# Kernel optimization log

Measured on AMD Instinct MI355X. Metric: run time of the kernel, lower is better.

Reference implementation:

```python
import jax, jax.numpy as jnp
import numpy as np

B = 4
N_CPGS = 20000
N_FREQS = N_CPGS // 2 + 1  # rfft length
E = 320000
H = 4
HD = 16          # head_dim = graph_hidden // n_heads
GH = 64          # graph_hidden
FD = 64          # fusion_dim
FH = 128         # fft_hidden
PH = 128         # plasticity_hidden


def _ln(x, g, b, eps=1e-5):
    m = x.mean(-1, keepdims=True)
    v = ((x - m) ** 2).mean(-1, keepdims=True)
    return (x - m) / jnp.sqrt(v + eps) * g + b


def _gelu(x):
    return jax.nn.gelu(x, approximate=False)  # torch default: exact erf GELU


def setup_inputs() -> dict:
    key = jax.random.key(0)
    ki = iter(jax.random.split(key, 40))
    nrm = lambda shape, s=0.02: jax.random.normal(next(ki), shape, dtype=jnp.float32) * s
    z = lambda *s: jnp.zeros(s, jnp.float32)
    o = lambda *s: jnp.ones(s, jnp.float32)
    return dict(
        x=jax.random.uniform(next(ki), (B, N_CPGS), dtype=jnp.float32),
        edge_index=jax.random.randint(next(ki), (2, E), 0, N_CPGS, dtype=jnp.int32),
        fft_freq_weights=o(N_FREQS),
        fft_w1=nrm((FH, N_FREQS)), fft_b1=z(FH), fft_ln1_g=o(FH), fft_ln1_b=z(FH),
        fft_w2=nrm((FD, FH)), fft_b2=z(FD), fft_ln2_g=o(FD), fft_ln2_b=z(FD),
        ge_w=nrm((GH, 1)), ge_b=z(GH), ge_ln_g=o(GH), ge_ln_b=z(GH),
        gat_w=nrm((GH, GH)), gat_attn=nrm((H, 2 * HD), 0.1),
        gp_w=nrm((FD, GH)), gp_b=z(FD), gp_ln_g=o(FD), gp_ln_b=z(FD),
        pl_W=nrm((PH, N_FREQS), 0.01), pl_alpha=o(PH, N_FREQS) * 0.01,
        pl_eta=jnp.array([0.1], jnp.float32), pl_bias=z(PH),
        pn_g=o(PH), pn_b=z(PH),
        pp_w=nrm((FD, PH)), pp_b=z(FD), pp_ln_g=o(FD), pp_ln_b=z(FD),
        gate_w1=nrm((6, 3 * FD)), gate_b1=z(6), gate_w2=nrm((3, 6)), gate_b2=z(3),
        head_w1=nrm((32, FD)), head_b1=z(32), head_w2=nrm((1, 32)), head_b2=z(1),
    )


def reference(x, edge_index, fft_freq_weights,
              fft_w1, fft_b1, fft_ln1_g, fft_ln1_b, fft_w2, fft_b2, fft_ln2_g, fft_ln2_b,
              ge_w, ge_b, ge_ln_g, ge_ln_b, gat_w, gat_attn,
              gp_w, gp_b, gp_ln_g, gp_ln_b,
              pl_W, pl_alpha, pl_eta, pl_bias, pn_g, pn_b,
              pp_w, pp_b, pp_ln_g, pp_ln_b,
              gate_w1, gate_b1, gate_w2, gate_b2,
              head_w1, head_b1, head_w2, head_b2):
    Bsz, n = x.shape
    # ---- Stream 1: FFT ----
    xc = x - x.mean(axis=1, keepdims=True)
    mag = jnp.log1p(jnp.abs(jnp.fft.rfft(xc, axis=1)))          # (B, N_FREQS)
    freq_w = jax.nn.softmax(fft_freq_weights) * fft_freq_weights.shape[0]
    magw = mag * freq_w[None, :]
    f = _gelu(_ln(magw @ fft_w1.T + fft_b1, fft_ln1_g, fft_ln1_b))
    fft_feat = _ln(f @ fft_w2.T + fft_b2, fft_ln2_g, fft_ln2_b)  # (B, FD)
    # ---- Stream 2: sparse graph attention (eval: dropout off) ----
    h0 = _gelu(_ln(x[..., None] * ge_w[:, 0] + ge_b, ge_ln_g, ge_ln_b))  # (B, N, GH)
    h = (h0 @ gat_w.T).reshape(Bsz, n, H, HD)
    a_src, a_dst = gat_attn[:, :HD], gat_attn[:, HD:]
    s_src = jnp.einsum('bnhd,hd->bnh', h, a_src)
    s_dst = jnp.einsum('bnhd,hd->bnh', h, a_dst)
    src, dst = edge_index[0], edge_index[1]
    scores = s_src[:, src] + s_dst[:, dst]                       # (B, E, H)
    scores = jnp.where(scores >= 0, scores, 0.2 * scores)        # leaky_relu(0.2)
    # max with include_self=True over zero-init buffer (matches torch scatter_reduce)
    m = jnp.zeros((Bsz, n, H), scores.dtype).at[:, dst].max(scores)
    e = jnp.exp(scores - m[:, dst])
    ssum = jnp.zeros((Bsz, n, H), e.dtype).at[:, dst].add(e)
    attn = e / (ssum[:, dst] + 1e-8)
    msg = h[:, src] * attn[..., None]                            # (B, E, H, HD)
    gat_out = jnp.zeros((Bsz, n, H, HD), msg.dtype).at[:, dst].add(msg).reshape(Bsz, n, H * HD)
    hg = h0 + _gelu(gat_out)
    graph_feat = _ln(hg.mean(axis=1) @ gp_w.T + gp_b, gp_ln_g, gp_ln_b)  # (B, FD)
    # ---- Stream 3: Hebbian plastic layer on mag ----
    y_slow = mag @ pl_W.T + pl_bias                              # (B, PH)
    x_norm = mag / (jnp.linalg.norm(mag, axis=-1, keepdims=True) + 1e-8)
    y_pre = jnp.tanh(y_slow)
    # bmm(alpha * eta * outer(y_pre, x_norm), x) == eta * y_pre * ((x_norm*x) @ alpha.T)
    contrib = pl_eta[0] * y_pre * ((x_norm * mag) @ jax.nn.sigmoid(pl_alpha).T)
    plastic = _ln(_gelu(y_slow + contrib), pn_g, pn_b)
    plastic_feat = _ln(plastic @ pp_w.T + pp_b, pp_ln_g, pp_ln_b)
    # ---- Gated fusion ----
    concat = jnp.concatenate([fft_feat, graph_feat, plastic_feat], axis=-1)  # (B, 3*FD)
    g = _gelu(concat @ gate_w1.T + gate_b1) @ gate_w2.T + gate_b2
    gw = jax.nn.softmax(g, axis=-1)                              # (B, 3)
    fused = fft_feat * gw[:, 0:1] + graph_feat * gw[:, 1:2] + plastic_feat * gw[:, 2:3]
    # ---- Head ----
    out = _gelu(fused @ head_w1.T + head_b1) @ head_w2.T + head_b2
    return out.squeeze(-1)                                       # (B,)
```

## Files before the change

kernel.cpp:

```cpp
#include <hip/hip_runtime.h>
#include <math.h>

constexpr int N_CPGS = 20000;
constexpr int NF     = 10001;
constexpr int BZ     = 4;
constexpr int NEDGE  = 320000;
constexpr int KPAD   = 10240;
constexpr int FN1    = 200;
constexpr int FN2    = 100;
constexpr int NS2    = 4;
constexpr int TILES  = (N_CPGS + 63) / 64;
constexpr int HB     = NEDGE / 256;

constexpr size_t W_XMEAN   = 0;
constexpr size_t W_SMSTAT  = 64;
constexpr size_t W_NORMSQ  = 128;
constexpr size_t W_H0SUM   = 192;
constexpr size_t W_GATMEAN = 448;
constexpr size_t W_PREP    = 704;
constexpr size_t W_D       = 768;
constexpr size_t W_MAG     = 2304;
constexpr size_t W_SSRC    = 42368;
constexpr size_t W_SDST    = 362368;
constexpr size_t W_H       = 682368;
constexpr size_t W_Y       = 5802368;
constexpr size_t W_P2      = 5962368;
constexpr size_t W_COUNTS  = 9079168;
constexpr size_t W_OFFS    = 9099168;
constexpr size_t W_CURSOR  = 9119232;
constexpr size_t W_SORTSRC = 9139232;

#define DEVFN static __device__ __forceinline__

DEVFN float gelu_f(float v) {
    float ax = fabsf(v) * 0.70710678118654752440f;
    float t = 1.0f / fmaf(0.3275911f, ax, 1.0f);
    float p = fmaf(t, 1.061405429f, -1.453152027f);
    p = fmaf(p, t, 1.421413741f);
    p = fmaf(p, t, -0.284496736f);
    p = fmaf(p, t, 0.254829592f);
    p = p * t;
    float e = __expf(-ax * ax);
    float er = copysignf(fmaf(-p, e, 1.0f), v);
    return 0.5f * v * (1.0f + er);
}

DEVFN float wred_sum(float v) {
    #pragma unroll
    for (int m = 32; m; m >>= 1) v += __shfl_xor(v, m);
    return v;
}

DEVFN unsigned int bfr(float f) {
    unsigned int u = __float_as_uint(f);
    return (u + 0x7fffu + ((u >> 16) & 1u)) >> 16;
}
DEVFN float bf2f(unsigned short v) { return __uint_as_float(((unsigned int)v) << 16); }

__global__ void k_pre(const float* __restrict__ x, const float* __restrict__ ge_w,
                      const float* __restrict__ ge_b, const float* __restrict__ fw,
                      float* __restrict__ ws) {
    int bb = blockIdx.x, t = threadIdx.x;
    __shared__ float sd[256];
    if (bb < 4) {
        const float4* x4 = (const float4*)(x + (size_t)bb * N_CPGS);
        float s = 0.f;
        for (int i = t; i < N_CPGS / 4; i += 256) {
            float4 v = x4[i];
            s += (v.x + v.y) + (v.z + v.w);
        }
        sd[t] = s; __syncthreads();
        for (int o = 128; o; o >>= 1) { if (t < o) sd[t] += sd[t + o]; __syncthreads(); }
        if (t == 0) ws[W_XMEAN + bb] = sd[0] * (1.0f / N_CPGS);
    } else if (bb == 4) {
        for (int i = t; i < (int)(W_PREP - W_NORMSQ); i += 256) ws[W_NORMSQ + i] = 0.f;
        if (t < 64) {
            float w = ge_w[t], b = ge_b[t];
            float mw = wred_sum(w) * (1.f / 64.f);
            float mb = wred_sum(b) * (1.f / 64.f);
            float wc = w - mw, bc = b - mb;
            float A = wred_sum(wc * wc) * (1.f / 64.f);
            float C = wred_sum(wc * bc) * (1.f / 64.f);
            float D = wred_sum(bc * bc) * (1.f / 64.f);
            if (t == 0) { float* p = ws + W_PREP; p[0] = mw; p[1] = mb; p[2] = A; p[3] = C; p[4] = D; }
        }
    } else if (bb == 5) {
        float mx = -1e30f;
        for (int i = t; i < NF; i += 256) mx = fmaxf(mx, fw[i]);
        sd[t] = mx; __syncthreads();
        for (int o = 128; o; o >>= 1) { if (t < o) sd[t] = fmaxf(sd[t], sd[t + o]); __syncthreads(); }
        mx = sd[0]; __syncthreads();
        float s = 0.f;
        for (int i = t; i < NF; i += 256) s += expf(fw[i] - mx);
        sd[t] = s; __syncthreads();
        for (int o = 128; o; o >>= 1) { if (t < o) sd[t] += sd[t + o]; __syncthreads(); }
        if (t == 0) { ws[W_SMSTAT] = mx; ws[W_SMSTAT + 1] = sd[0]; }
    } else {
        int base = (bb - 6) * 1000;
        int* cnt = (int*)(ws + W_COUNTS);
        for (int i = t; i < 1000; i += 256) cnt[base + i] = 0;
    }
}

__global__ __launch_bounds__(256) void k_node(
    const float* __restrict__ x, const float* __restrict__ ge_w, const float* __restrict__ ge_b,
    const float* __restrict__ ge_g, const float* __restrict__ ge_beta,
    const float* __restrict__ gat_w, const float* __restrict__ gat_attn,
    const int* __restrict__ ei, float* __restrict__ ws)
{
    int t = threadIdx.x;
    int nb = blockIdx.x;
    if (nb >= 4 * TILES) {
        int r = nb - 4 * TILES;
        if (r < HB) {
            int e = r * 256 + t;
            if (e < NEDGE) atomicAdd((int*)(ws + W_COUNTS) + ei[NEDGE + e], 1);
        } else {
            int fb = r - HB;
            int b = fb / 100;
            int n1base = (fb % 100) * 2;
            int n1l = t >> 7, k2 = t & 127;
            __shared__ float xs[2][100];
            float xm = ws[W_XMEAN + b];
            for (int i = t; i < 200; i += 256) {
                int nl = (i >= 100) ? 1 : 0, n2 = (i >= 100) ? i - 100 : i;
                xs[nl][n2] = x[(size_t)b * N_CPGS + n1base + nl + 200 * n2] - xm;
            }
            __syncthreads();
            int k2e = (k2 < 100) ? k2 : 0;
            constexpr float T100 = 6.2831853071795864769f / 100.f;
            float dc, dsn;
            { float sn, cn; sincosf(T100 * (float)k2e, &sn, &cn); dc = cn; dsn = -sn; }
            float yr = 0.f, yi = 0.f;
            #pragma unroll
            for (int half = 0; half < 2; ++half) {
                float c, s;
                { int m = (k2e * (half * 50)) % 100; float sn, cn; sincosf(T100 * (float)m, &sn, &cn); c = cn; s = -sn; }
                #pragma unroll 5
                for (int j = 0; j < 50; ++j) {
                    float xv = xs[n1l][half * 50 + j];
                    yr = fmaf(xv, c, yr); yi = fmaf(xv, s, yi);
                    float tc_ = c * dc - s * dsn; s = s * dc + c * dsn; c = tc_;
                }
            }
            if (k2 < 100)
                ((float2*)(ws + W_Y))[((size_t)b * FN1 + n1base + n1l) * FN2 + k2] = make_float2(yr, yi);
        }
        return;
    }
    int b = nb / TILES;
    int tile = nb % TILES;
    int n0 = tile * 64;

    __shared__ __align__(16) float h0T[64 * 68];
    __shared__ __align__(16) float gwT[64 * 68];
    __shared__ float xsv[64], rss[64];

    const float* prep = ws + W_PREP;
    float mw = prep[0], mb = prep[1], A = prep[2], C = prep[3], Dd = prep[4];

    for (int idx = t; idx < 4096; idx += 256) { int i = idx >> 6, j = idx & 63; gwT[j * 68 + i] = gat_w[idx]; }
    if (t < 64) {
        int n = n0 + t;
        float xv = (n < N_CPGS) ? x[(size_t)b * N_CPGS + n] : 0.f;
        xsv[t] = xv;
        float var = xv * xv * A + 2.f * xv * C + Dd;
        rss[t] = 1.0f / sqrtf(var + 1e-5f);
    }
    __syncthreads();

    for (int idx = t; idx < 4096; idx += 256) {
        int j = idx >> 6, nd = idx & 63;
        float h0 = 0.f;
        if (n0 + nd < N_CPGS) {
            float v = (xsv[nd] * (ge_w[j] - mw) + (ge_b[j] - mb)) * rss[nd];
            h0 = gelu_f(v * ge_g[j] + ge_beta[j]);
        }
        h0T[j * 68 + nd] = h0;
    }
    __syncthreads();

    int tr = t >> 4, tc = t & 15;
    float acc[4][4] = {};
    #pragma unroll 8
    for (int j = 0; j < 64; ++j) {
        const float4 av = *(const float4*)&h0T[j * 68 + (tr << 2)];
        const float4 bv = *(const float4*)&gwT[j * 68 + (tc << 2)];
        #pragma unroll
        for (int u = 0; u < 4; ++u) {
            float a = (u == 0) ? av.x : (u == 1) ? av.y : (u == 2) ? av.z : av.w;
            acc[u][0] = fmaf(a, bv.x, acc[u][0]);
            acc[u][1] = fmaf(a, bv.y, acc[u][1]);
            acc[u][2] = fmaf(a, bv.z, acc[u][2]);
            acc[u][3] = fmaf(a, bv.w, acc[u][3]);
        }
    }
    if (t < 64) {
        float s = 0.f;
        #pragma unroll 8
        for (int nd = 0; nd < 64; ++nd) s += h0T[t * 68 + nd];
        atomicAdd(ws + W_H0SUM + b * 64 + t, s);
    }
    unsigned short* hb = (unsigned short*)(ws + W_H);
    #pragma unroll
    for (int u = 0; u < 4; ++u) {
        int n = n0 + tr * 4 + u;
        if (n < N_CPGS) {
            unsigned int lo = bfr(acc[u][0]) | (bfr(acc[u][1]) << 16);
            unsigned int hi = bfr(acc[u][2]) | (bfr(acc[u][3]) << 16);
            *(uint2*)(hb + ((size_t)b * N_CPGS + n) * 64 + tc * 4) = make_uint2(lo, hi);
        }
    }
    __syncthreads();
    #pragma unroll
    for (int u = 0; u < 4; ++u)
        *(float4*)&h0T[(tr * 4 + u) * 68 + tc * 4] =
            make_float4(acc[u][0], acc[u][1], acc[u][2], acc[u][3]);
    __syncthreads();
    if (t < 64) {
        int n = n0 + t;
        if (n < N_CPGS) {
            #pragma unroll
            for (int hh = 0; hh < 4; ++hh) {
                float as = 0.f, ad = 0.f;
                #pragma unroll
                for (int d = 0; d < 16; ++d) {
                    float hv = h0T[t * 68 + hh * 16 + d];
                    as = fmaf(hv, gat_attn[hh * 32 + d], as);
                    ad = fmaf(hv, gat_attn[hh * 32 + 16 + d], ad);
                }
                ws[W_SSRC + ((size_t)b * N_CPGS + n) * 4 + hh] = as;
                ws[W_SDST + ((size_t)b * N_CPGS + n) * 4 + hh] = ad;
            }
        }
    }
}

__global__ __launch_bounds__(1024) void k_sf2(float* __restrict__ ws) {
    int t = threadIdx.x;
    if (blockIdx.x == 0) {
        const int* cnt = (const int*)(ws + W_COUNTS);
        int* offs = (int*)(ws + W_OFFS);
        int* cur  = (int*)(ws + W_CURSOR);
        int i0 = t * 20;
        int s = 0;
        for (int i = 0; i < 20; ++i) { int idx = i0 + i; if (idx < N_CPGS) s += cnt[idx]; }
        __shared__ int sd[1024];
        sd[t] = s; __syncthreads();
        for (int off = 1; off < 1024; off <<= 1) {
            int v = (t >= off) ? sd[t - off] : 0;
            __syncthreads();
            sd[t] += v;
            __syncthreads();
        }
        int run = sd[t] - s;
        for (int i = 0; i < 20; ++i) {
            int idx = i0 + i;
            if (idx < N_CPGS) { offs[idx] = run; cur[idx] = run; run += cnt[idx]; }
        }
        if (t == 1023) offs[N_CPGS] = sd[1023];
        return;
    }
    int kb = blockIdx.x - 1;
    int ns = t >> 8;
    int k = kb * 256 + (t & 255);
    int n1b = ns * 50;
    int k2 = k % 100;
    const float2* Y2 = (const float2*)(ws + W_Y);
    constexpr float W0 = 6.2831853071795864769f / 20000.f;
    float dc, dsn;
    { float sn, cn; sincosf(W0 * (float)k, &sn, &cn); dc = cn; dsn = -sn; }
    float c, s;
    { int m = (k * n1b) % 20000; float sn, cn; sincosf(W0 * (float)m, &sn, &cn); c = cn; s = -sn; }
    float xr0 = 0.f, xi0 = 0.f, xr1 = 0.f, xi1 = 0.f;
    float xr2 = 0.f, xi2 = 0.f, xr3 = 0.f, xi3 = 0.f;
    #pragma unroll 5
    for (int j = 0; j < 50; ++j) {
        int n1 = n1b + j;
        float2 y0 = Y2[(0 * FN1 + (size_t)n1) * FN2 + k2];
        float2 y1 = Y2[(1 * FN1 + (size_t)n1) * FN2 + k2];
        float2 y2 = Y2[(2 * FN1 + (size_t)n1) * FN2 + k2];
        float2 y3 = Y2[(3 * FN1 + (size_t)n1) * FN2 + k2];
        xr0 = fmaf(y0.x, c, xr0); xr0 = fmaf(-y0.y, s, xr0);
        xi0 = fmaf(y0.x, s, xi0); xi0 = fmaf( y0.y, c, xi0);
        xr1 = fmaf(y1.x, c, xr1); xr1 = fmaf(-y1.y, s, xr1);
        xi1 = fmaf(y1.x, s, xi1); xi1 = fmaf( y1.y, c, xi1);
        xr2 = fmaf(y2.x, c, xr2); xr2 = fmaf(-y2.y, s, xr2);
        xi2 = fmaf(y2.x, s, xi2); xi2 = fmaf( y2.y, c, xi2);
        xr3 = fmaf(y3.x, c, xr3); xr3 = fmaf(-y3.y, s, xr3);
        xi3 = fmaf(y3.x, s, xi3); xi3 = fmaf( y3.y, c, xi3);
        float tc_ = c * dc - s * dsn; s = s * dc + c * dsn; c = tc_;
    }
    float* p = ws + W_P2 + ((size_t)ns * KPAD + k) * 8;
    p[0] = xr0; p[1] = xi0; p[2] = xr1; p[3] = xi1;
    p[4] = xr2; p[5] = xi2; p[6] = xr3; p[7] = xi3;
}

__global__ __launch_bounds__(256) void k_scatmagr(const int* __restrict__ ei,
                                                  float* __restrict__ ws) {
    int t = threadIdx.x;
    if (blockIdx.x < HB) {
        int e = blockIdx.x * 256 + t;
        if (e < NEDGE) {
            int s = ei[e], d = ei[NEDGE + e];
            int pos = atomicAdd((int*)(ws + W_CURSOR) + d, 1);
            ((int*)(ws + W_SORTSRC))[pos] = s;
        }
        return;
    }
    int gid = (blockIdx.x - HB) * 256 + t;
    bool ok = gid < BZ * NF;
    int b = ok ? gid / NF : 0;
    int k = ok ? gid - b * NF : 0;
    float m = 0.f;
    if (ok) {
        float re = 0.f, im = 0.f;
        const float* p = ws + W_P2 + (size_t)k * 8 + b * 2;
        #pragma unroll
        for (int ns = 0; ns < NS2; ++ns) { re += p[0]; im += p[1]; p += (size_t)KPAD * 8; }
        m = log1pf(sqrtf(re * re + im * im));
        ws[W_MAG + (size_t)b * NF + k] = m;
    }
    float msq = ok ? m * m : 0.f;
    #pragma unroll
    for (int bb = 0; bb < 4; ++bb) {
        float v = (ok && b == bb) ? msq : 0.f;
        v = wred_sum(v);
        if ((t & 63) == 0) atomicAdd(ws + W_NORMSQ + bb, v);
    }
}

__global__ __launch_bounds__(256) void k_gatdots(
    const float* __restrict__ fftw1, const float* __restrict__ plW,
    const float* __restrict__ plalpha, const float* __restrict__ fw,
    float* __restrict__ ws)
{
    int t = threadIdx.x;
    if (blockIdx.x < 2048) {
        int xcd = blockIdx.x & 7;
        int b = xcd >> 1;
        int blk = ((blockIdx.x >> 3) << 1) | (xcd & 1);
        int w = t >> 6, lane = t & 63;
        int wv = blk * 4 + w;
        int egrp = lane >> 4, fgrp = lane & 15;
        int hh = fgrp >> 2;
        const int* offs = (const int*)(ws + W_OFFS);
        const int* ssrt = (const int*)(ws + W_SORTSRC);
        const float4* s4src = (const float4*)(ws + W_SSRC);
        const float4* s4dst = (const float4*)(ws + W_SDST);
        const unsigned short* hb = (const unsigned short*)(ws + W_H);
        size_t bN = (size_t)b * N_CPGS;
        float gacc0 = 0.f, gacc1 = 0.f, gacc2 = 0.f, gacc3 = 0.f;

        __shared__ float elds[4][4][68];
        __shared__ int   slds[4][68];

        for (int dst = wv; dst < N_CPGS; dst += 2048) {
            int o0 = offs[dst], o1 = offs[dst + 1];
            if (o0 == o1) continue;
            float4 sd4 = s4dst[bN + dst];
            float p0 = 0.f, p1 = 0.f, p2 = 0.f, p3 = 0.f;
            float a0 = 0.f, a1 = 0.f, a2 = 0.f, a3 = 0.f;
            for (int c0 = o0; c0 < o1; c0 += 64) {
                int cnt = min(64, o1 - c0);
                float v0 = 0.f, v1 = 0.f, v2 = 0.f, v3 = 0.f;
                int s = 0;
                if (lane < cnt) {
                    s = ssrt[c0 + lane];
                    float4 ss = s4src[bN + s];
                    v0 = ss.x + sd4.x; v0 = (v0 >= 0.f) ? v0 : 0.2f * v0; v0 = __expf(v0);
                    v1 = ss.y + sd4.y; v1 = (v1 >= 0.f) ? v1 : 0.2f * v1; v1 = __expf(v1);
                    v2 = ss.z + sd4.z; v2 = (v2 >= 0.f) ? v2 : 0.2f * v2; v2 = __expf(v2);
                    v3 = ss.w + sd4.w; v3 = (v3 >= 0.f) ? v3 : 0.2f * v3; v3 = __expf(v3);
                }
                slds[w][lane] = s;
                elds[w][0][lane] = v0; elds[w][1][lane] = v1;
                elds[w][2][lane] = v2; elds[w][3][lane] = v3;
                p0 += v0; p1 += v1; p2 += v2; p3 += v3;
                int niter = (cnt + 3) >> 2;
                for (int i = 0; i < niter; ++i) {
                    int j = i * 4 + egrp;
                    float e = elds[w][hh][j];
                    int sj = slds[w][j];
                    uint2 hv = *(const uint2*)(hb + (((size_t)(bN + sj)) << 6) + (fgrp << 2));
                    a0 = fmaf(e, bf2f((unsigned short)(hv.x & 0xffffu)), a0);
                    a1 = fmaf(e, bf2f((unsigned short)(hv.x >> 16)), a1);
                    a2 = fmaf(e, bf2f((unsigned short)(hv.y & 0xffffu)), a2);
                    a3 = fmaf(e, bf2f((unsigned short)(hv.y >> 16)), a3);
                }
            }
            float q0 = wred_sum(p0), q1 = wred_sum(p1), q2 = wred_sum(p2), q3 = wred_sum(p3);
            float ssum = (hh == 0) ? q0 : (hh == 1) ? q1 : (hh == 2) ? q2 : q3;
            a0 += __shfl_xor(a0, 16); a0 += __shfl_xor(a0, 32);
            a1 += __shfl_xor(a1, 16); a1 += __shfl_xor(a1, 32);
            a2 += __shfl_xor(a2, 16); a2 += __shfl_xor(a2, 32);
            a3 += __shfl_xor(a3, 16); a3 += __shfl_xor(a3, 32);
            float inv = 1.f / (ssum + 1e-8f);
            gacc0 += gelu_f(a0 * inv); gacc1 += gelu_f(a1 * inv);
            gacc2 += gelu_f(a2 * inv); gacc3 += gelu_f(a3 * inv);
        }
        __shared__ float gred[4][64];
        if (egrp == 0) {
            gred[w][fgrp * 4 + 0] = gacc0; gred[w][fgrp * 4 + 1] = gacc1;
            gred[w][fgrp * 4 + 2] = gacc2; gred[w][fgrp * 4 + 3] = gacc3;
        }
        __syncthreads();
        if (t < 64)
            atomicAdd(ws + W_GATMEAN + b * 64 + t, gred[0][t] + gred[1][t] + gred[2][t] + gred[3][t]);
        return;
    }
    int bb2 = blockIdx.x - 2048;
    int m = bb2 >> 7;
    int r = bb2 & 127;
    const float* mag = ws + W_MAG;
    float smx = ws[W_SMSTAT], ssm = ws[W_SMSTAT + 1];
    float sc_fw = (float)NF / ssm;
    float inv_n0 = 1.f / (sqrtf(ws[W_NORMSQ + 0]) + 1e-8f);
    float inv_n1 = 1.f / (sqrtf(ws[W_NORMSQ + 1]) + 1e-8f);
    float inv_n2 = 1.f / (sqrtf(ws[W_NORMSQ + 2]) + 1e-8f);
    float inv_n3 = 1.f / (sqrtf(ws[W_NORMSQ + 3]) + 1e-8f);
    const float* row = ((m == 0) ? fftw1 : (m == 1) ? plW : plalpha) + (size_t)r * NF;
    float a0 = 0.f, a1 = 0.f, a2 = 0.f, a3 = 0.f;
    for (int k = t; k < NF; k += 256) {
        float wv = row[k];
        float g0 = mag[k], g1 = mag[NF + k], g2 = mag[2 * NF + k], g3 = mag[3 * NF + k];
        if (m == 0) {
            float s = expf(fw[k] - smx) * sc_fw;
            wv *= s;
            a0 = fmaf(wv, g0, a0); a1 = fmaf(wv, g1, a1); a2 = fmaf(wv, g2, a2); a3 = fmaf(wv, g3, a3);
        } else if (m == 1) {
            a0 = fmaf(wv, g0, a0); a1 = fmaf(wv, g1, a1); a2 = fmaf(wv, g2, a2); a3 = fmaf(wv, g3, a3);
        } else {
            wv = 1.f / (1.f + expf(-wv));
            a0 = fmaf(wv, g0 * g0 * inv_n0, a0); a1 = fmaf(wv, g1 * g1 * inv_n1, a1);
            a2 = fmaf(wv, g2 * g2 * inv_n2, a2); a3 = fmaf(wv, g3 * g3 * inv_n3, a3);
        }
    }
    __shared__ float sd[256];
    float acc[4] = {a0, a1, a2, a3};
    #pragma unroll
    for (int bb = 0; bb < 4; ++bb) {
        sd[t] = acc[bb]; __syncthreads();
        for (int o = 128; o; o >>= 1) { if (t < o) sd[t] += sd[t + o]; __syncthreads(); }
        if (t == 0) ws[W_D + ((size_t)m * 128 + r) * 4 + bb] = sd[0];
        __syncthreads();
    }
}

DEVFN float ln64(float v, const float* g, const float* bt, int lane) {
    float mn = wred_sum(v) * (1.f / 64.f);
    float d = v - mn;
    float var = wred_sum(d * d) * (1.f / 64.f);
    return d * (1.0f / sqrtf(var + 1e-5f)) * g[lane] + bt[lane];
}
DEVFN void ln128(float& v0, float& v1, const float* g, const float* bt, int lane) {
    float mn = wred_sum(v0 + v1) * (1.f / 128.f);
    float d0 = v0 - mn, d1 = v1 - mn;
    float var = wred_sum(d0 * d0 + d1 * d1) * (1.f / 128.f);
    float rs = 1.0f / sqrtf(var + 1e-5f);
    v0 = d0 * rs * g[lane] + bt[lane];
    v1 = d1 * rs * g[lane + 64] + bt[lane + 64];
}
DEVFN float dotW128(const float* __restrict__ W, const float* __restrict__ v, int c) {
    const float4* w4 = (const float4*)(W + (size_t)c * 128);
    float acc = 0.f;
    #pragma unroll
    for (int q = 0; q < 32; ++q) {
        float4 wv = w4[q];
        const float* vv = v + q * 4;
        acc = fmaf(wv.x, vv[0], acc); acc = fmaf(wv.y, vv[1], acc);
        acc = fmaf(wv.z, vv[2], acc); acc = fmaf(wv.w, vv[3], acc);
    }
    return acc;
}
DEVFN float dotW64(const float* __restrict__ W, const float* __restrict__ v, int c) {
    const float4* w4 = (const float4*)(W + (size_t)c * 64);
    float acc = 0.f;
    #pragma unroll
    for (int q = 0; q < 16; ++q) {
        float4 wv = w4[q];
        const float* vv = v + q * 4;
        acc = fmaf(wv.x, vv[0], acc); acc = fmaf(wv.y, vv[1], acc);
        acc = fmaf(wv.z, vv[2], acc); acc = fmaf(wv.w, vv[3], acc);
    }
    return acc;
}

__global__ __launch_bounds__(256) void k_final(
    const float* __restrict__ fft_b1, const float* __restrict__ fft_ln1_g, const float* __restrict__ fft_ln1_b,
    const float* __restrict__ fft_w2, const float* __restrict__ fft_b2,
    const float* __restrict__ fft_ln2_g, const float* __restrict__ fft_ln2_b,
    const float* __restrict__ gp_w, const float* __restrict__ gp_b,
    const float* __restrict__ gp_ln_g, const float* __restrict__ gp_ln_b,
    const float* __restrict__ pl_eta, const float* __restrict__ pl_bias,
    const float* __restrict__ pn_g, const float* __restrict__ pn_b,
    const float* __restrict__ pp_w, const float* __restrict__ pp_b,
    const float* __restrict__ pp_ln_g, const float* __restrict__ pp_ln_b,
    const float* __restrict__ gate_w1, const float* __restrict__ gate_b1,
    const float* __restrict__ gate_w2, const float* __restrict__ gate_b2,
    const float* __restrict__ head_w1, const float* __restrict__ head_b1,
    const float* __restrict__ head_w2, const float* __restrict__ head_b2,
    float* __restrict__ ws, float* __restrict__ out)
{
    int t = threadIdx.x, b = t >> 6, lane = t & 63;
    __shared__ float vlds[4][256];
    float* vb = vlds[b];
    const float* D = ws + W_D;
    int r0 = lane, r1 = lane + 64;

    float f0 = D[(0 * 128 + r0) * 4 + b] + fft_b1[r0];
    float f1 = D[(0 * 128 + r1) * 4 + b] + fft_b1[r1];
    ln128(f0, f1, fft_ln1_g, fft_ln1_b, lane);
    vb[lane] = gelu_f(f0); vb[64 + lane] = gelu_f(f1);
    float catf = ln64(dotW128(fft_w2, vb, lane) + fft_b2[lane], fft_ln2_g, fft_ln2_b, lane);

    float hgm = (ws[W_H0SUM + b * 64 + lane] + ws[W_GATMEAN + b * 64 + lane]) * (1.f / N_CPGS);
    vb[lane] = hgm;
    float catg = ln64(dotW64(gp_w, vb, lane) + gp_b[lane], gp_ln_g, gp_ln_b, lane);

    float eta = pl_eta[0];
    float ys0 = D[(1 * 128 + r0) * 4 + b] + pl_bias[r0];
    float ys1 = D[(1 * 128 + r1) * 4 + b] + pl_bias[r1];
    float q0 = D[(2 * 128 + r0) * 4 + b];
    float q1 = D[(2 * 128 + r1) * 4 + b];
    float u0 = gelu_f(ys0 + eta * tanhf(ys0) * q0);
    float u1 = gelu_f(ys1 + eta * tanhf(ys1) * q1);
    ln128(u0, u1, pn_g, pn_b, lane);
    vb[lane] = u0; vb[64 + lane] = u1;
    float catp = ln64(dotW128(pp_w, vb, lane) + pp_b[lane], pp_ln_g, pp_ln_b, lane);

    vb[lane] = catf; vb[64 + lane] = catg; vb[128 + lane] = catp;
    if (lane < 6) {
        float a = gate_b1[lane];
        const float* wrow = gate_w1 + lane * 192;
        #pragma unroll 4
        for (int j = 0; j < 192; ++j) a = fmaf(wrow[j], vb[j], a);
        vb[192 + lane] = gelu_f(a);
    }
    float gv[3];
    #pragma unroll
    for (int c = 0; c < 3; ++c) {
        float a = gate_b2[c];
        #pragma unroll
        for (int j = 0; j < 6; ++j) a = fmaf(gate_w2[c * 6 + j], vb[192 + j], a);
        gv[c] = a;
    }
    float gmx = fmaxf(gv[0], fmaxf(gv[1], gv[2]));
    float e0 = expf(gv[0] - gmx), e1 = expf(gv[1] - gmx), e2 = expf(gv[2] - gmx);
    float inv = 1.f / (e0 + e1 + e2);
    float fus = catf * (e0 * inv) + catg * (e1 * inv) + catp * (e2 * inv);

    vb[lane] = fus;
    float hval = 0.f;
    if (lane < 32) {
        float a = dotW64(head_w1, vb, lane) + head_b1[lane];
        hval = gelu_f(a) * head_w2[lane];
    }
    float o = wred_sum(hval);
    if (lane == 0) out[b] = o + head_b2[0];
}

extern "C" void kernel_launch(void* const* d_in, const int* in_sizes, int n_in,
                              void* d_out, int out_size, void* d_ws, size_t ws_size,
                              hipStream_t stream) {
    (void)in_sizes; (void)n_in; (void)out_size; (void)ws_size;
    const float* x        = (const float*)d_in[0];
    const int*   ei       = (const int*)d_in[1];
    const float* fw       = (const float*)d_in[2];
    const float* fft_w1   = (const float*)d_in[3];
    const float* fft_b1   = (const float*)d_in[4];
    const float* fft_ln1g = (const float*)d_in[5];
    const float* fft_ln1b = (const float*)d_in[6];
    const float* fft_w2   = (const float*)d_in[7];
    const float* fft_b2   = (const float*)d_in[8];
    const float* fft_ln2g = (const float*)d_in[9];
    const float* fft_ln2b = (const float*)d_in[10];
    const float* ge_w     = (const float*)d_in[11];
    const float* ge_b     = (const float*)d_in[12];
    const float* ge_g     = (const float*)d_in[13];
    const float* ge_beta  = (const float*)d_in[14];
    const float* gat_w    = (const float*)d_in[15];
    const float* gat_attn = (const float*)d_in[16];
    const float* gp_w     = (const float*)d_in[17];
    const float* gp_b     = (const float*)d_in[18];
    const float* gp_ln_g  = (const float*)d_in[19];
    const float* gp_ln_b  = (const float*)d_in[20];
    const float* pl_W     = (const float*)d_in[21];
    const float* pl_alpha = (const float*)d_in[22];
    const float* pl_eta   = (const float*)d_in[23];
    const float* pl_bias  = (const float*)d_in[24];
    const float* pn_g     = (const float*)d_in[25];
    const float* pn_b     = (const float*)d_in[26];
    const float* pp_w     = (const float*)d_in[27];
    const float* pp_b     = (const float*)d_in[28];
    const float* pp_ln_g  = (const float*)d_in[29];
    const float* pp_ln_b  = (const float*)d_in[30];
    const float* gate_w1  = (const float*)d_in[31];
    const float* gate_b1  = (const float*)d_in[32];
    const float* gate_w2  = (const float*)d_in[33];
    const float* gate_b2  = (const float*)d_in[34];
    const float* head_w1  = (const float*)d_in[35];
    const float* head_b1  = (const float*)d_in[36];
    const float* head_w2  = (const float*)d_in[37];
    const float* head_b2  = (const float*)d_in[38];

    float* ws  = (float*)d_ws;
    float* out = (float*)d_out;

    k_pre<<<26, 256, 0, stream>>>(x, ge_w, ge_b, fw, ws);
    k_node<<<4 * TILES + HB + 400, 256, 0, stream>>>(x, ge_w, ge_b, ge_g, ge_beta,
                                                     gat_w, gat_attn, ei, ws);
    k_sf2<<<41, 1024, 0, stream>>>(ws);
    k_scatmagr<<<HB + (BZ * NF + 255) / 256, 256, 0, stream>>>(ei, ws);
    k_gatdots<<<2048 + 384, 256, 0, stream>>>(fft_w1, pl_W, pl_alpha, fw, ws);
    k_final<<<1, 256, 0, stream>>>(fft_b1, fft_ln1g, fft_ln1b, fft_w2, fft_b2, fft_ln2g, fft_ln2b,
                                   gp_w, gp_b, gp_ln_g, gp_ln_b, pl_eta, pl_bias, pn_g, pn_b,
                                   pp_w, pp_b, pp_ln_g, pp_ln_b, gate_w1, gate_b1, gate_w2, gate_b2,
                                   head_w1, head_b1, head_w2, head_b2, ws, out);
}
```

Before: 213.9 us.

## Interleave batch dimension in node/FFT buffers and process all batches per GAT destination

Changes the layouts of the FFT intermediate Y, the bf16 node features H and the attention scores so the batch index is innermost. This lets the second FFT stage read all four batches with two float4 loads and the GAT aggregation handle all four batches per destination in one pass. Edge indices and the softmax setup are then shared across batches instead of repeated. The attention score dot products are now computed from registers with lane shuffles instead of a shared-memory round trip. The FFT second stage is split over eight n1 segments with twice the blocks. The price is much higher register use per GAT thread and fewer GAT blocks.

```diff
diff --git a/kernel.cpp b/kernel.cpp
--- a/kernel.cpp
+++ b/kernel.cpp
@@ -8,9 +8,10 @@
 constexpr int KPAD   = 10240;
 constexpr int FN1    = 200;
 constexpr int FN2    = 100;
-constexpr int NS2    = 4;
+constexpr int NS2    = 8;
 constexpr int TILES  = (N_CPGS + 63) / 64;
 constexpr int HB     = NEDGE / 256;
+constexpr int GATB   = 1024;
 
 constexpr size_t W_XMEAN   = 0;
 constexpr size_t W_SMSTAT  = 64;
@@ -144,7 +145,7 @@
                 }
             }
             if (k2 < 100)
-                ((float2*)(ws + W_Y))[((size_t)b * FN1 + n1base + n1l) * FN2 + k2] = make_float2(yr, yi);
+                ((float2*)(ws + W_Y))[((size_t)(n1base + n1l) * FN2 + k2) * 4 + b] = make_float2(yr, yi);
         }
         return;
     }
@@ -201,36 +202,44 @@
         for (int nd = 0; nd < 64; ++nd) s += h0T[t * 68 + nd];
         atomicAdd(ws + W_H0SUM + b * 64 + t, s);
     }
-    unsigned short* hb = (unsigned short*)(ws + W_H);
+    unsigned short* hbp = (unsigned short*)(ws + W_H);
     #pragma unroll
     for (int u = 0; u < 4; ++u) {
         int n = n0 + tr * 4 + u;
         if (n < N_CPGS) {
             unsigned int lo = bfr(acc[u][0]) | (bfr(acc[u][1]) << 16);
             unsigned int hi = bfr(acc[u][2]) | (bfr(acc[u][3]) << 16);
-            *(uint2*)(hb + ((size_t)b * N_CPGS + n) * 64 + tc * 4) = make_uint2(lo, hi);
-        }
-    }
-    __syncthreads();
-    #pragma unroll
-    for (int u = 0; u < 4; ++u)
-        *(float4*)&h0T[(tr * 4 + u) * 68 + tc * 4] =
-            make_float4(acc[u][0], acc[u][1], acc[u][2], acc[u][3]);
-    __syncthreads();
-    if (t < 64) {
-        int n = n0 + t;
-        if (n < N_CPGS) {
+            *(uint2*)(hbp + ((size_t)n * 4 + b) * 64 + tc * 4) = make_uint2(lo, hi);
+        }
+    }
+    {
+        int hh = tc >> 2;
+        float ps[4], pd[4];
+        #pragma unroll
+        for (int u = 0; u < 4; ++u) {
+            float s = 0.f, d = 0.f;
             #pragma unroll
-            for (int hh = 0; hh < 4; ++hh) {
-                float as = 0.f, ad = 0.f;
-                #pragma unroll
-                for (int d = 0; d < 16; ++d) {
-                    float hv = h0T[t * 68 + hh * 16 + d];
-                    as = fmaf(hv, gat_attn[hh * 32 + d], as);
-                    ad = fmaf(hv, gat_attn[hh * 32 + 16 + d], ad);
+            for (int kk = 0; kk < 4; ++kk) {
+                float asv = gat_attn[hh * 32 + (tc & 3) * 4 + kk];
+                float adv = gat_attn[hh * 32 + 16 + (tc & 3) * 4 + kk];
+                s = fmaf(acc[u][kk], asv, s);
+                d = fmaf(acc[u][kk], adv, d);
+            }
+            ps[u] = s; pd[u] = d;
+        }
+        #pragma unroll
+        for (int u = 0; u < 4; ++u) {
+            ps[u] += __shfl_xor(ps[u], 1); ps[u] += __shfl_xor(ps[u], 2);
+            pd[u] += __shfl_xor(pd[u], 1); pd[u] += __shfl_xor(pd[u], 2);
+        }
+        if ((tc & 3) == 0) {
+            #pragma unroll
+            for (int u = 0; u < 4; ++u) {
+                int n = n0 + tr * 4 + u;
+                if (n < N_CPGS) {
+                    ws[W_SSRC + ((size_t)n * 4 + b) * 4 + hh] = ps[u];
+                    ws[W_SDST + ((size_t)n * 4 + b) * 4 + hh] = pd[u];
                 }
-                ws[W_SSRC + ((size_t)b * N_CPGS + n) * 4 + hh] = as;
-                ws[W_SDST + ((size_t)b * N_CPGS + n) * 4 + hh] = ad;
             }
         }
     }
@@ -261,12 +270,13 @@
         if (t == 1023) offs[N_CPGS] = sd[1023];
         return;
     }
-    int kb = blockIdx.x - 1;
-    int ns = t >> 8;
+    int bb = blockIdx.x - 1;
+    int kb = bb >> 1;
+    int ns = (bb & 1) * 4 + (t >> 8);
     int k = kb * 256 + (t & 255);
-    int n1b = ns * 50;
+    int n1b = ns * 25;
     int k2 = k % 100;
-    const float2* Y2 = (const float2*)(ws + W_Y);
+    const float4* Yp = (const float4*)(ws + W_Y);
     constexpr float W0 = 6.2831853071795864769f / 20000.f;
     float dc, dsn;
     { float sn, cn; sincosf(W0 * (float)k, &sn, &cn); dc = cn; dsn = -sn; }
@@ -275,20 +285,17 @@
     float xr0 = 0.f, xi0 = 0.f, xr1 = 0.f, xi1 = 0.f;
     float xr2 = 0.f, xi2 = 0.f, xr3 = 0.f, xi3 = 0.f;
     #pragma unroll 5
-    for (int j = 0; j < 50; ++j) {
-        int n1 = n1b + j;
-        float2 y0 = Y2[(0 * FN1 + (size_t)n1) * FN2 + k2];
-        float2 y1 = Y2[(1 * FN1 + (size_t)n1) * FN2 + k2];
-        float2 y2 = Y2[(2 * FN1 + (size_t)n1) * FN2 + k2];
-        float2 y3 = Y2[(3 * FN1 + (size_t)n1) * FN2 + k2];
-        xr0 = fmaf(y0.x, c, xr0); xr0 = fmaf(-y0.y, s, xr0);
-        xi0 = fmaf(y0.x, s, xi0); xi0 = fmaf( y0.y, c, xi0);
-        xr1 = fmaf(y1.x, c, xr1); xr1 = fmaf(-y1.y, s, xr1);
-        xi1 = fmaf(y1.x, s, xi1); xi1 = fmaf( y1.y, c, xi1);
-        xr2 = fmaf(y2.x, c, xr2); xr2 = fmaf(-y2.y, s, xr2);
-        xi2 = fmaf(y2.x, s, xi2); xi2 = fmaf( y2.y, c, xi2);
-        xr3 = fmaf(y3.x, c, xr3); xr3 = fmaf(-y3.y, s, xr3);
-        xi3 = fmaf(y3.x, s, xi3); xi3 = fmaf( y3.y, c, xi3);
+    for (int j = 0; j < 25; ++j) {
+        size_t base = ((size_t)(n1b + j) * FN2 + k2) * 2;
+        float4 y01 = Yp[base], y23 = Yp[base + 1];
+        xr0 = fmaf(y01.x, c, xr0); xr0 = fmaf(-y01.y, s, xr0);
+        xi0 = fmaf(y01.x, s, xi0); xi0 = fmaf( y01.y, c, xi0);
+        xr1 = fmaf(y01.z, c, xr1); xr1 = fmaf(-y01.w, s, xr1);
+        xi1 = fmaf(y01.z, s, xi1); xi1 = fmaf( y01.w, c, xi1);
+        xr2 = fmaf(y23.x, c, xr2); xr2 = fmaf(-y23.y, s, xr2);
+        xi2 = fmaf(y23.x, s, xi2); xi2 = fmaf( y23.y, c, xi2);
+        xr3 = fmaf(y23.z, c, xr3); xr3 = fmaf(-y23.w, s, xr3);
+        xi3 = fmaf(y23.z, s, xi3); xi3 = fmaf( y23.w, c, xi3);
         float tc_ = c * dc - s * dsn; s = s * dc + c * dsn; c = tc_;
     }
     float* p = ws + W_P2 + ((size_t)ns * KPAD + k) * 8;
@@ -336,80 +343,106 @@
     float* __restrict__ ws)
 {
     int t = threadIdx.x;
-    if (blockIdx.x < 2048) {
-        int xcd = blockIdx.x & 7;
-        int b = xcd >> 1;
-        int blk = ((blockIdx.x >> 3) << 1) | (xcd & 1);
+    if (blockIdx.x < GATB) {
         int w = t >> 6, lane = t & 63;
-        int wv = blk * 4 + w;
+        int wv = blockIdx.x * 4 + w;
         int egrp = lane >> 4, fgrp = lane & 15;
         int hh = fgrp >> 2;
         const int* offs = (const int*)(ws + W_OFFS);
         const int* ssrt = (const int*)(ws + W_SORTSRC);
         const float4* s4src = (const float4*)(ws + W_SSRC);
         const float4* s4dst = (const float4*)(ws + W_SDST);
-        const unsigned short* hb = (const unsigned short*)(ws + W_H);
-        size_t bN = (size_t)b * N_CPGS;
-        float gacc0 = 0.f, gacc1 = 0.f, gacc2 = 0.f, gacc3 = 0.f;
-
-        __shared__ float elds[4][4][68];
+        const uint2* hbp = (const uint2*)(ws + W_H);
+        float gacc[4][4] = {};
+
+        __shared__ float elds[4][4][4][68];
         __shared__ int   slds[4][68];
-
-        for (int dst = wv; dst < N_CPGS; dst += 2048) {
+        __shared__ float gred[4][4][64];
+
+        for (int dst = wv; dst < N_CPGS; dst += 4 * GATB) {
             int o0 = offs[dst], o1 = offs[dst + 1];
             if (o0 == o1) continue;
-            float4 sd4 = s4dst[bN + dst];
-            float p0 = 0.f, p1 = 0.f, p2 = 0.f, p3 = 0.f;
-            float a0 = 0.f, a1 = 0.f, a2 = 0.f, a3 = 0.f;
+            float4 sd4[4];
+            #pragma unroll
+            for (int b = 0; b < 4; ++b) sd4[b] = s4dst[(size_t)dst * 4 + b];
+            float av[4][4] = {};
+            float es[4] = {};
             for (int c0 = o0; c0 < o1; c0 += 64) {
                 int cnt = min(64, o1 - c0);
-                float v0 = 0.f, v1 = 0.f, v2 = 0.f, v3 = 0.f;
                 int s = 0;
-                if (lane < cnt) {
-                    s = ssrt[c0 + lane];
-                    float4 ss = s4src[bN + s];
-                    v0 = ss.x + sd4.x; v0 = (v0 >= 0.f) ? v0 : 0.2f * v0; v0 = __expf(v0);
-                    v1 = ss.y + sd4.y; v1 = (v1 >= 0.f) ? v1 : 0.2f * v1; v1 = __expf(v1);
-                    v2 = ss.z + sd4.z; v2 = (v2 >= 0.f) ? v2 : 0.2f * v2; v2 = __expf(v2);
-                    v3 = ss.w + sd4.w; v3 = (v3 >= 0.f) ? v3 : 0.2f * v3; v3 = __expf(v3);
+                if (lane < cnt) s = ssrt[c0 + lane];
+                slds[w][lane] = s;
+                #pragma unroll
+                for (int b = 0; b < 4; ++b) {
+                    float v0 = 0.f, v1 = 0.f, v2 = 0.f, v3 = 0.f;
+                    if (lane < cnt) {
+                        float4 ss = s4src[(size_t)s * 4 + b];
+                        v0 = ss.x + sd4[b].x; v0 = (v0 >= 0.f) ? v0 : 0.2f * v0; v0 = __expf(v0);
+                        v1 = ss.y + sd4[b].y; v1 = (v1 >= 0.f) ? v1 : 0.2f * v1; v1 = __expf(v1);
+                        v2 = ss.z + sd4[b].z; v2 = (v2 >= 0.f) ? v2 : 0.2f * v2; v2 = __expf(v2);
+                        v3 = ss.w + sd4[b].w; v3 = (v3 >= 0.f) ? v3 : 0.2f * v3; v3 = __expf(v3);
+                    }
+                    elds[w][b][0][lane] = v0; elds[w][b][1][lane] = v1;
+                    elds[w][b][2][lane] = v2; elds[w][b][3][lane] = v3;
                 }
-                slds[w][lane] = s;
-                elds[w][0][lane] = v0; elds[w][1][lane] = v1;
-                elds[w][2][lane] = v2; elds[w][3][lane] = v3;
-                p0 += v0; p1 += v1; p2 += v2; p3 += v3;
                 int niter = (cnt + 3) >> 2;
                 for (int i = 0; i < niter; ++i) {
-                    int j = i * 4 + egrp;
-                    float e = elds[w][hh][j];
+                    int j = (i << 2) + egrp;
                     int sj = slds[w][j];
-                    uint2 hv = *(const uint2*)(hb + (((size_t)(bN + sj)) << 6) + (fgrp << 2));
-                    a0 = fmaf(e, bf2f((unsigned short)(hv.x & 0xffffu)), a0);
-                    a1 = fmaf(e, bf2f((unsigned short)(hv.x >> 16)), a1);
-                    a2 = fmaf(e, bf2f((unsigned short)(hv.y & 0xffffu)), a2);
-                    a3 = fmaf(e, bf2f((unsigned short)(hv.y >> 16)), a3);
+                    const uint2* hp = hbp + (size_t)sj * 64 + fgrp;
+                    float e0 = elds[w][0][hh][j];
+                    float e1 = elds[w][1][hh][j];
+                    float e2 = elds[w][2][hh][j];
+                    float e3 = elds[w][3][hh][j];
+                    uint2 h0 = hp[0], h1 = hp[16], h2 = hp[32], h3 = hp[48];
+                    es[0] += e0; es[1] += e1; es[2] += e2; es[3] += e3;
+                    av[0][0] = fmaf(e0, bf2f((unsigned short)(h0.x & 0xffffu)), av[0][0]);
+                    av[0][1] = fmaf(e0, bf2f((unsigned short)(h0.x >> 16)),     av[0][1]);
+                    av[0][2] = fmaf(e0, bf2f((unsigned short)(h0.y & 0xffffu)), av[0][2]);
+                    av[0][3] = fmaf(e0, bf2f((unsigned short)(h0.y >> 16)),     av[0][3]);
+                    av[1][0] = fmaf(e1, bf2f((unsigned short)(h1.x & 0xffffu)), av[1][0]);
+                    av[1][1] = fmaf(e1, bf2f((unsigned short)(h1.x >> 16)),     av[1][1]);
+                    av[1][2] = fmaf(e1, bf2f((unsigned short)(h1.y & 0xffffu)), av[1][2]);
+                    av[1][3] = fmaf(e1, bf2f((unsigned short)(h1.y >> 16)),     av[1][3]);
+                    av[2][0] = fmaf(e2, bf2f((unsigned short)(h2.x & 0xffffu)), av[2][0]);
+                    av[2][1] = fmaf(e2, bf2f((unsigned short)(h2.x >> 16)),     av[2][1]);
+                    av[2][2] = fmaf(e2, bf2f((unsigned short)(h2.y & 0xffffu)), av[2][2]);
+                    av[2][3] = fmaf(e2, bf2f((unsigned short)(h2.y >> 16)),     av[2][3]);
+                    av[3][0] = fmaf(e3, bf2f((unsigned short)(h3.x & 0xffffu)), av[3][0]);
+                    av[3][1] = fmaf(e3, bf2f((unsigned short)(h3.x >> 16)),     av[3][1]);
+                    av[3][2] = fmaf(e3, bf2f((unsigned short)(h3.y & 0xffffu)), av[3][2]);
+                    av[3][3] = fmaf(e3, bf2f((unsigned short)(h3.y >> 16)),     av[3][3]);
                 }
             }
-            float q0 = wred_sum(p0), q1 = wred_sum(p1), q2 = wred_sum(p2), q3 = wred_sum(p3);
-            float ssum = (hh == 0) ? q0 : (hh == 1) ? q1 : (hh == 2) ? q2 : q3;
-            a0 += __shfl_xor(a0, 16); a0 += __shfl_xor(a0, 32);
-            a1 += __shfl_xor(a1, 16); a1 += __shfl_xor(a1, 32);
-            a2 += __shfl_xor(a2, 16); a2 += __shfl_xor(a2, 32);
-            a3 += __shfl_xor(a3, 16); a3 += __shfl_xor(a3, 32);
-            float inv = 1.f / (ssum + 1e-8f);
-            gacc0 += gelu_f(a0 * inv); gacc1 += gelu_f(a1 * inv);
-            gacc2 += gelu_f(a2 * inv); gacc3 += gelu_f(a3 * inv);
-        }
-        __shared__ float gred[4][64];
+            #pragma unroll
+            for (int b = 0; b < 4; ++b) {
+                float sden = es[b];
+                sden += __shfl_xor(sden, 16); sden += __shfl_xor(sden, 32);
+                float inv = 1.f / (sden + 1e-8f);
+                #pragma unroll
+                for (int k = 0; k < 4; ++k) {
+                    float a = av[b][k];
+                    a += __shfl_xor(a, 16); a += __shfl_xor(a, 32);
+                    gacc[b][k] += gelu_f(a * inv);
+                }
+            }
+        }
         if (egrp == 0) {
-            gred[w][fgrp * 4 + 0] = gacc0; gred[w][fgrp * 4 + 1] = gacc1;
-            gred[w][fgrp * 4 + 2] = gacc2; gred[w][fgrp * 4 + 3] = gacc3;
+            #pragma unroll
+            for (int b = 0; b < 4; ++b)
+                #pragma unroll
+                for (int k = 0; k < 4; ++k)
+                    gred[w][b][fgrp * 4 + k] = gacc[b][k];
         }
         __syncthreads();
-        if (t < 64)
-            atomicAdd(ws + W_GATMEAN + b * 64 + t, gred[0][t] + gred[1][t] + gred[2][t] + gred[3][t]);
+        {
+            int b = t >> 6, f = t & 63;
+            atomicAdd(ws + W_GATMEAN + b * 64 + f,
+                      gred[0][b][f] + gred[1][b][f] + gred[2][b][f] + gred[3][b][f]);
+        }
         return;
     }
-    int bb2 = blockIdx.x - 2048;
+    int bb2 = blockIdx.x - GATB;
     int m = bb2 >> 7;
     int r = bb2 & 127;
     const float* mag = ws + W_MAG;
@@ -610,9 +643,9 @@
     k_pre<<<26, 256, 0, stream>>>(x, ge_w, ge_b, fw, ws);
     k_node<<<4 * TILES + HB + 400, 256, 0, stream>>>(x, ge_w, ge_b, ge_g, ge_beta,
                                                      gat_w, gat_attn, ei, ws);
-    k_sf2<<<41, 1024, 0, stream>>>(ws);
+    k_sf2<<<81, 1024, 0, stream>>>(ws);
     k_scatmagr<<<HB + (BZ * NF + 255) / 256, 256, 0, stream>>>(ei, ws);
-    k_gatdots<<<2048 + 384, 256, 0, stream>>>(fft_w1, pl_W, pl_alpha, fw, ws);
+    k_gatdots<<<GATB + 384, 256, 0, stream>>>(fft_w1, pl_W, pl_alpha, fw, ws);
     k_final<<<1, 256, 0, stream>>>(fft_b1, fft_ln1g, fft_ln1b, fft_w2, fft_b2, fft_ln2g, fft_ln2b,
                                    gp_w, gp_b, gp_ln_g, gp_ln_b, pl_eta, pl_bias, pn_g, pn_b,
                                    pp_w, pp_b, pp_ln_g, pp_ln_b, gate_w1, gate_b1, gate_w2, gate_b2,
```

Result: slower. 226.1 us (+5.7%).

## Split DFT stage two across more blocks, interleave batch layout, compute attention scores in registers

Applied to the files above, without the earlier changes.

The second DFT stage now splits the n1 reduction into 8 slices instead of 4, doubling the block count. The intermediate Y buffer is stored batch-interleaved so each thread loads two float4s per step instead of four scattered float2s. Node attention scores are computed directly from the GEMM accumulators with lane shuffles, dropping a shared-memory round trip and two barriers. The GAT aggregation accumulates the softmax denominator per lane instead of running four full-wave reductions, and the dot-product blocks are scheduled before the edge blocks. The cost is more partial sums for the downstream combine step.

```diff
diff --git a/kernel.cpp b/kernel.cpp
--- a/kernel.cpp
+++ b/kernel.cpp
@@ -8,9 +8,10 @@
 constexpr int KPAD   = 10240;
 constexpr int FN1    = 200;
 constexpr int FN2    = 100;
-constexpr int NS2    = 4;
+constexpr int NS2    = 8;
 constexpr int TILES  = (N_CPGS + 63) / 64;
 constexpr int HB     = NEDGE / 256;
+constexpr int DOTSB  = 384;
 
 constexpr size_t W_XMEAN   = 0;
 constexpr size_t W_SMSTAT  = 64;
@@ -144,7 +145,7 @@
                 }
             }
             if (k2 < 100)
-                ((float2*)(ws + W_Y))[((size_t)b * FN1 + n1base + n1l) * FN2 + k2] = make_float2(yr, yi);
+                ((float2*)(ws + W_Y))[((size_t)(n1base + n1l) * FN2 + k2) * 4 + b] = make_float2(yr, yi);
         }
         return;
     }
@@ -201,36 +202,44 @@
         for (int nd = 0; nd < 64; ++nd) s += h0T[t * 68 + nd];
         atomicAdd(ws + W_H0SUM + b * 64 + t, s);
     }
-    unsigned short* hb = (unsigned short*)(ws + W_H);
+    unsigned short* hbp = (unsigned short*)(ws + W_H);
     #pragma unroll
     for (int u = 0; u < 4; ++u) {
         int n = n0 + tr * 4 + u;
         if (n < N_CPGS) {
             unsigned int lo = bfr(acc[u][0]) | (bfr(acc[u][1]) << 16);
             unsigned int hi = bfr(acc[u][2]) | (bfr(acc[u][3]) << 16);
-            *(uint2*)(hb + ((size_t)b * N_CPGS + n) * 64 + tc * 4) = make_uint2(lo, hi);
-        }
-    }
-    __syncthreads();
-    #pragma unroll
-    for (int u = 0; u < 4; ++u)
-        *(float4*)&h0T[(tr * 4 + u) * 68 + tc * 4] =
-            make_float4(acc[u][0], acc[u][1], acc[u][2], acc[u][3]);
-    __syncthreads();
-    if (t < 64) {
-        int n = n0 + t;
-        if (n < N_CPGS) {
+            *(uint2*)(hbp + ((size_t)b * N_CPGS + n) * 64 + tc * 4) = make_uint2(lo, hi);
+        }
+    }
+    {
+        int hh = tc >> 2;
+        float ps[4], pd[4];
+        #pragma unroll
+        for (int u = 0; u < 4; ++u) {
+            float s = 0.f, d = 0.f;
             #pragma unroll
-            for (int hh = 0; hh < 4; ++hh) {
-                float as = 0.f, ad = 0.f;
-                #pragma unroll
-                for (int d = 0; d < 16; ++d) {
-                    float hv = h0T[t * 68 + hh * 16 + d];
-                    as = fmaf(hv, gat_attn[hh * 32 + d], as);
-                    ad = fmaf(hv, gat_attn[hh * 32 + 16 + d], ad);
+            for (int kk = 0; kk < 4; ++kk) {
+                float asv = gat_attn[hh * 32 + (tc & 3) * 4 + kk];
+                float adv = gat_attn[hh * 32 + 16 + (tc & 3) * 4 + kk];
+                s = fmaf(acc[u][kk], asv, s);
+                d = fmaf(acc[u][kk], adv, d);
+            }
+            ps[u] = s; pd[u] = d;
+        }
+        #pragma unroll
+        for (int u = 0; u < 4; ++u) {
+            ps[u] += __shfl_xor(ps[u], 1); ps[u] += __shfl_xor(ps[u], 2);
+            pd[u] += __shfl_xor(pd[u], 1); pd[u] += __shfl_xor(pd[u], 2);
+        }
+        if ((tc & 3) == 0) {
+            #pragma unroll
+            for (int u = 0; u < 4; ++u) {
+                int n = n0 + tr * 4 + u;
+                if (n < N_CPGS) {
+                    ws[W_SSRC + ((size_t)b * N_CPGS + n) * 4 + hh] = ps[u];
+                    ws[W_SDST + ((size_t)b * N_CPGS + n) * 4 + hh] = pd[u];
                 }
-                ws[W_SSRC + ((size_t)b * N_CPGS + n) * 4 + hh] = as;
-                ws[W_SDST + ((size_t)b * N_CPGS + n) * 4 + hh] = ad;
             }
         }
     }
@@ -261,12 +270,13 @@
         if (t == 1023) offs[N_CPGS] = sd[1023];
         return;
     }
-    int kb = blockIdx.x - 1;
-    int ns = t >> 8;
+    int bb = blockIdx.x - 1;
+    int kb = bb >> 1;
+    int ns = (bb & 1) * 4 + (t >> 8);
     int k = kb * 256 + (t & 255);
-    int n1b = ns * 50;
+    int n1b = ns * 25;
     int k2 = k % 100;
-    const float2* Y2 = (const float2*)(ws + W_Y);
+    const float4* Yp = (const float4*)(ws + W_Y);
     constexpr float W0 = 6.2831853071795864769f / 20000.f;
     float dc, dsn;
     { float sn, cn; sincosf(W0 * (float)k, &sn, &cn); dc = cn; dsn = -sn; }
@@ -275,20 +285,17 @@
     float xr0 = 0.f, xi0 = 0.f, xr1 = 0.f, xi1 = 0.f;
     float xr2 = 0.f, xi2 = 0.f, xr3 = 0.f, xi3 = 0.f;
     #pragma unroll 5
-    for (int j = 0; j < 50; ++j) {
-        int n1 = n1b + j;
-        float2 y0 = Y2[(0 * FN1 + (size_t)n1) * FN2 + k2];
-        float2 y1 = Y2[(1 * FN1 + (size_t)n1) * FN2 + k2];
-        float2 y2 = Y2[(2 * FN1 + (size_t)n1) * FN2 + k2];
-        float2 y3 = Y2[(3 * FN1 + (size_t)n1) * FN2 + k2];
-        xr0 = fmaf(y0.x, c, xr0); xr0 = fmaf(-y0.y, s, xr0);
-        xi0 = fmaf(y0.x, s, xi0); xi0 = fmaf( y0.y, c, xi0);
-        xr1 = fmaf(y1.x, c, xr1); xr1 = fmaf(-y1.y, s, xr1);
-        xi1 = fmaf(y1.x, s, xi1); xi1 = fmaf( y1.y, c, xi1);
-        xr2 = fmaf(y2.x, c, xr2); xr2 = fmaf(-y2.y, s, xr2);
-        xi2 = fmaf(y2.x, s, xi2); xi2 = fmaf( y2.y, c, xi2);
-        xr3 = fmaf(y3.x, c, xr3); xr3 = fmaf(-y3.y, s, xr3);
-        xi3 = fmaf(y3.x, s, xi3); xi3 = fmaf( y3.y, c, xi3);
+    for (int j = 0; j < 25; ++j) {
+        size_t base = ((size_t)(n1b + j) * FN2 + k2) * 2;
+        float4 y01 = Yp[base], y23 = Yp[base + 1];
+        xr0 = fmaf(y01.x, c, xr0); xr0 = fmaf(-y01.y, s, xr0);
+        xi0 = fmaf(y01.x, s, xi0); xi0 = fmaf( y01.y, c, xi0);
+        xr1 = fmaf(y01.z, c, xr1); xr1 = fmaf(-y01.w, s, xr1);
+        xi1 = fmaf(y01.z, s, xi1); xi1 = fmaf( y01.w, c, xi1);
+        xr2 = fmaf(y23.x, c, xr2); xr2 = fmaf(-y23.y, s, xr2);
+        xi2 = fmaf(y23.x, s, xi2); xi2 = fmaf( y23.y, c, xi2);
+        xr3 = fmaf(y23.z, c, xr3); xr3 = fmaf(-y23.w, s, xr3);
+        xi3 = fmaf(y23.z, s, xi3); xi3 = fmaf( y23.w, c, xi3);
         float tc_ = c * dc - s * dsn; s = s * dc + c * dsn; c = tc_;
     }
     float* p = ws + W_P2 + ((size_t)ns * KPAD + k) * 8;
@@ -336,10 +343,11 @@
     float* __restrict__ ws)
 {
     int t = threadIdx.x;
-    if (blockIdx.x < 2048) {
-        int xcd = blockIdx.x & 7;
+    if (blockIdx.x >= DOTSB) {
+        int g = blockIdx.x - DOTSB;
+        int xcd = g & 7;
         int b = xcd >> 1;
-        int blk = ((blockIdx.x >> 3) << 1) | (xcd & 1);
+        int blk = ((g >> 3) << 1) | (xcd & 1);
         int w = t >> 6, lane = t & 63;
         int wv = blk * 4 + w;
         int egrp = lane >> 4, fgrp = lane & 15;
@@ -348,18 +356,19 @@
         const int* ssrt = (const int*)(ws + W_SORTSRC);
         const float4* s4src = (const float4*)(ws + W_SSRC);
         const float4* s4dst = (const float4*)(ws + W_SDST);
-        const unsigned short* hb = (const unsigned short*)(ws + W_H);
+        const uint2* hbp = (const uint2*)(ws + W_H);
         size_t bN = (size_t)b * N_CPGS;
         float gacc0 = 0.f, gacc1 = 0.f, gacc2 = 0.f, gacc3 = 0.f;
 
         __shared__ float elds[4][4][68];
         __shared__ int   slds[4][68];
+        __shared__ float gred[4][64];
 
         for (int dst = wv; dst < N_CPGS; dst += 2048) {
             int o0 = offs[dst], o1 = offs[dst + 1];
             if (o0 == o1) continue;
             float4 sd4 = s4dst[bN + dst];
-            float p0 = 0.f, p1 = 0.f, p2 = 0.f, p3 = 0.f;
+            float es = 0.f;
             float a0 = 0.f, a1 = 0.f, a2 = 0.f, a3 = 0.f;
             for (int c0 = o0; c0 < o1; c0 += 64) {
                 int cnt = min(64, o1 - c0);
@@ -376,30 +385,28 @@
                 slds[w][lane] = s;
                 elds[w][0][lane] = v0; elds[w][1][lane] = v1;
                 elds[w][2][lane] = v2; elds[w][3][lane] = v3;
-                p0 += v0; p1 += v1; p2 += v2; p3 += v3;
                 int niter = (cnt + 3) >> 2;
                 for (int i = 0; i < niter; ++i) {
-                    int j = i * 4 + egrp;
+                    int j = (i << 2) + egrp;
                     float e = elds[w][hh][j];
                     int sj = slds[w][j];
-                    uint2 hv = *(const uint2*)(hb + (((size_t)(bN + sj)) << 6) + (fgrp << 2));
+                    uint2 hv = hbp[(bN + sj) * 16 + fgrp];
+                    es += e;
                     a0 = fmaf(e, bf2f((unsigned short)(hv.x & 0xffffu)), a0);
-                    a1 = fmaf(e, bf2f((unsigned short)(hv.x >> 16)), a1);
+                    a1 = fmaf(e, bf2f((unsigned short)(hv.x >> 16)),     a1);
                     a2 = fmaf(e, bf2f((unsigned short)(hv.y & 0xffffu)), a2);
-                    a3 = fmaf(e, bf2f((unsigned short)(hv.y >> 16)), a3);
+                    a3 = fmaf(e, bf2f((unsigned short)(hv.y >> 16)),     a3);
                 }
             }
-            float q0 = wred_sum(p0), q1 = wred_sum(p1), q2 = wred_sum(p2), q3 = wred_sum(p3);
-            float ssum = (hh == 0) ? q0 : (hh == 1) ? q1 : (hh == 2) ? q2 : q3;
+            es += __shfl_xor(es, 16); es += __shfl_xor(es, 32);
             a0 += __shfl_xor(a0, 16); a0 += __shfl_xor(a0, 32);
             a1 += __shfl_xor(a1, 16); a1 += __shfl_xor(a1, 32);
             a2 += __shfl_xor(a2, 16); a2 += __shfl_xor(a2, 32);
             a3 += __shfl_xor(a3, 16); a3 += __shfl_xor(a3, 32);
-            float inv = 1.f / (ssum + 1e-8f);
+            float inv = 1.f / (es + 1e-8f);
             gacc0 += gelu_f(a0 * inv); gacc1 += gelu_f(a1 * inv);
             gacc2 += gelu_f(a2 * inv); gacc3 += gelu_f(a3 * inv);
         }
-        __shared__ float gred[4][64];
         if (egrp == 0) {
             gred[w][fgrp * 4 + 0] = gacc0; gred[w][fgrp * 4 + 1] = gacc1;
             gred[w][fgrp * 4 + 2] = gacc2; gred[w][fgrp * 4 + 3] = gacc3;
@@ -409,7 +416,7 @@
             atomicAdd(ws + W_GATMEAN + b * 64 + t, gred[0][t] + gred[1][t] + gred[2][t] + gred[3][t]);
         return;
     }
-    int bb2 = blockIdx.x - 2048;
+    int bb2 = blockIdx.x;
     int m = bb2 >> 7;
     int r = bb2 & 127;
     const float* mag = ws + W_MAG;
@@ -610,9 +617,9 @@
     k_pre<<<26, 256, 0, stream>>>(x, ge_w, ge_b, fw, ws);
     k_node<<<4 * TILES + HB + 400, 256, 0, stream>>>(x, ge_w, ge_b, ge_g, ge_beta,
                                                      gat_w, gat_attn, ei, ws);
-    k_sf2<<<41, 1024, 0, stream>>>(ws);
+    k_sf2<<<81, 1024, 0, stream>>>(ws);
     k_scatmagr<<<HB + (BZ * NF + 255) / 256, 256, 0, stream>>>(ei, ws);
-    k_gatdots<<<2048 + 384, 256, 0, stream>>>(fft_w1, pl_W, pl_alpha, fw, ws);
+    k_gatdots<<<DOTSB + 2048, 256, 0, stream>>>(fft_w1, pl_W, pl_alpha, fw, ws);
     k_final<<<1, 256, 0, stream>>>(fft_b1, fft_ln1g, fft_ln1b, fft_w2, fft_b2, fft_ln2g, fft_ln2b,
                                    gp_w, gp_b, gp_ln_g, gp_ln_b, pl_eta, pl_bias, pn_g, pn_b,
                                    pp_w, pp_b, pp_ln_g, pp_ln_b, gate_w1, gate_b1, gate_w2, gate_b2,
```

New measurement: 214.0 us. Within noise of the previous version (+0.0%).
